# Kernel optimization log

Measured on AMD Instinct MI355X. Metric: run time of the kernel, lower is better.

## Reference

```python
import jax, jax.numpy as jnp
import numpy as np
import math

B, S, D, H = 4, 2048, 1024, 16
DH = D // H
NEG = -1e10


def setup_inputs() -> dict:
    key = jax.random.key(0)
    k1, k2, k3 = jax.random.split(key, 3)
    x = jax.random.normal(k1, (B, S, D), dtype=jnp.float32)
    # torch nn.Linear weights have shape (out_features, in_features); y = x @ W.T + b
    w1 = jax.random.normal(k2, (3 * D, D), dtype=jnp.float32) * (1.0 / math.sqrt(D))
    b1 = jnp.zeros((3 * D,), dtype=jnp.float32)
    w2 = jax.random.normal(k3, (D, D), dtype=jnp.float32) * (1.0 / math.sqrt(D))
    b2 = jnp.zeros((D,), dtype=jnp.float32)
    return {"x": x, "w1": w1, "b1": b1, "w2": w2, "b2": b2}


def reference(x, w1, b1, w2, b2):
    b, s, d = x.shape
    h, dh = H, d // H
    qkv = x @ w1.T + b1                                  # [B,S,3D]
    q, k, v = jnp.split(qkv, 3, axis=-1)                 # each [B,S,D]
    def heads(t):
        return t.reshape(b, s, h, dh).transpose(0, 2, 1, 3)  # [B,H,S,dh]
    q, k, v = heads(q), heads(k), heads(v)
    # additive causal mask: (1 - tril) * -1e10, as in the original
    mask = (1.0 - jnp.tril(jnp.ones((s, s), dtype=x.dtype))) * NEG
    scores = jnp.einsum('bhqd,bhkd->bhqk', q, k) / math.sqrt(dh) + mask
    attn = jax.nn.softmax(scores, axis=-1)
    o = jnp.einsum('bhqk,bhkd->bhqd', attn, v)           # [B,H,S,dh]
    o = o.transpose(0, 2, 1, 3).reshape(b, s, d)         # [B,S,D]
    return o @ w2.T + b2
```

## Files before the change

### kernel.cpp

```cpp
#include <hip/hip_runtime.h>
#include <stdint.h>


typedef __bf16 bf16;
typedef __attribute__((ext_vector_type(4))) __bf16 bf16x4;
typedef __attribute__((ext_vector_type(8))) __bf16 bf16x8;
typedef __attribute__((ext_vector_type(4))) float f32x4;

#define MFMA16(a, b, c) __builtin_amdgcn_mfma_f32_16x16x32_bf16((a), (b), (c), 0, 0, 0)

#if __has_builtin(__builtin_amdgcn_exp2f)
#define EXP2F(x) __builtin_amdgcn_exp2f(x)
#else
#define EXP2F(x) exp2f(x)
#endif

#define GLOAD_LDS16(gp, lp)                                                    \
  __builtin_amdgcn_global_load_lds(                                            \
      (__attribute__((address_space(1))) void*)(gp),                           \
      (__attribute__((address_space(3))) void*)(lp), 16, 0, 0)

#define SB   2048
#define D3   3072
#define DD   1024
#define QSCALE 0.18033688011112042f

__global__ __launch_bounds__(256) void cast_bf16_kernel(
    const float* __restrict__ in, bf16* __restrict__ out, int n4) {
  int stride = gridDim.x * blockDim.x;
  for (int i = blockIdx.x * blockDim.x + threadIdx.x; i < n4; i += stride) {
    float4 v = ((const float4*)in)[i];
    bf16x4 p;
    p[0] = (bf16)v.x; p[1] = (bf16)v.y; p[2] = (bf16)v.z; p[3] = (bf16)v.w;
    *(bf16x4*)(out + (size_t)i * 4) = p;
  }
}

template <int OUTMODE>
__global__ __launch_bounds__(256) void gemm_bt_kernel(
    const bf16* __restrict__ A, const bf16* __restrict__ Bw,
    const float* __restrict__ bias, void* __restrict__ Cout,
    int M, int N, int K) {
  __shared__ __attribute__((aligned(16))) bf16 At[128 * 32];
  __shared__ __attribute__((aligned(16))) bf16 Bt[128 * 32];
  const int tid = threadIdx.x;
  const int w = tid >> 6, l = tid & 63;
  const int c = l & 15, g = l >> 4;
  const int wm = w >> 1, wn = w & 1;
  const int m0 = blockIdx.y * 128, n0 = blockIdx.x * 128;

  const int srow = w * 32 + (l >> 2);
  const int scol = (l & 3) * 8;
  const bf16* Ag = A + (size_t)(m0 + srow) * K + scol;
  const bf16* Bg = Bw + (size_t)(n0 + srow) * K + scol;
  char* AtB = (char*)At + w * 2048;
  char* BtB = (char*)Bt + w * 2048;

  f32x4 acc[4][4] = {};

  for (int k0 = 0; k0 < K; k0 += 32) {
    GLOAD_LDS16(Ag + k0,            AtB);
    GLOAD_LDS16(Ag + 16 * K + k0,   AtB + 1024);
    GLOAD_LDS16(Bg + k0,            BtB);
    GLOAD_LDS16(Bg + 16 * K + k0,   BtB + 1024);
    __syncthreads();

    bf16x8 aF[4], bF[4];
    const char* Ard = (const char*)At + (wm * 64 + c) * 64 + g * 16;
    const char* Brd = (const char*)Bt + (wn * 64 + c) * 64 + g * 16;
#pragma unroll
    for (int mi = 0; mi < 4; ++mi) aF[mi] = *(const bf16x8*)(Ard + mi * 1024);
#pragma unroll
    for (int ni = 0; ni < 4; ++ni) bF[ni] = *(const bf16x8*)(Brd + ni * 1024);
#pragma unroll
    for (int mi = 0; mi < 4; ++mi)
#pragma unroll
      for (int ni = 0; ni < 4; ++ni)
        acc[mi][ni] = MFMA16(aF[mi], bF[ni], acc[mi][ni]);
    __syncthreads();
  }

#pragma unroll
  for (int ni = 0; ni < 4; ++ni) {
    const int col = n0 + wn * 64 + ni * 16 + c;
    const float bv = bias[col];
#pragma unroll
    for (int mi = 0; mi < 4; ++mi) {
      const int row = m0 + wm * 64 + mi * 16 + 4 * g;
#pragma unroll
      for (int r = 0; r < 4; ++r) {
        float v = acc[mi][ni][r] + bv;
        if (OUTMODE == 1) {
          if (col < DD) v *= QSCALE;
          ((bf16*)Cout)[(size_t)(row + r) * N + col] = (bf16)v;
        } else {
          ((float*)Cout)[(size_t)(row + r) * N + col] = v;
        }
      }
    }
  }
}

__global__ __launch_bounds__(256) void vtrans_kernel(
    const bf16* __restrict__ qkv, bf16* __restrict__ vT) {
  __shared__ __attribute__((aligned(16))) bf16 tt[64 * 72];
  const int tid = threadIdx.x;
  const int bh = blockIdx.x >> 5, st = blockIdx.x & 31;
  const int b = bh >> 4, h = bh & 15;
  const int s0 = st * 64;
  const int sr = tid >> 3, c0 = (tid & 7) * 8;
#pragma unroll
  for (int i = 0; i < 2; ++i) {
    const int srr = sr + i * 32;
    bf16x8 v = *(const bf16x8*)(qkv + (size_t)(b * SB + s0 + srr) * D3 + 2 * DD + h * 64 + c0);
    *(bf16x8*)(&tt[srr * 72 + c0]) = v;
  }
  __syncthreads();
  const int d = tid >> 2;
#pragma unroll
  for (int i = 0; i < 2; ++i) {
    const int sc = (tid & 3) * 2 + i;
    bf16x8 v;
#pragma unroll
    for (int j = 0; j < 8; ++j) v[j] = tt[(sc * 8 + j) * 72 + d];
    *(bf16x8*)(vT + (size_t)(bh * 64 + d) * SB + s0 + sc * 8) = v;
  }
}

__global__ __launch_bounds__(256, 2) void attn_kernel(
    const bf16* __restrict__ qkv, const bf16* __restrict__ vT,
    bf16* __restrict__ o) {
  __shared__ __attribute__((aligned(16))) bf16 Kt[2][128 * 64];
  __shared__ __attribute__((aligned(16))) bf16 Vt[2][64 * 128];
  const int tid = threadIdx.x;
  const int w = tid >> 6, l = tid & 63;
  const int c = l & 15, g = l >> 4;
  const int pair = blockIdx.x >> 6, bh = blockIdx.x & 63;
  const int b = bh >> 4, h = bh & 15;
  const int qtA = pair, qtB = 15 - pair;
  const int swz = (c & 7) << 4;

  const bf16* qg = qkv + (size_t)(b * SB) * D3 + h * 64;

  auto stage = [&](int kt, int buf) {
#pragma unroll
    for (int j = 0; j < 4; ++j) {
      const int row = w * 32 + j * 8 + (l >> 3);
      const int cs = ((l & 7) ^ (row & 7)) << 3;
      GLOAD_LDS16(qkv + (size_t)(b * SB + kt * 128 + row) * D3 + DD + h * 64 + cs,
                  (char*)&Kt[buf][0] + w * 4096 + j * 1024);
    }
#pragma unroll
    for (int j = 0; j < 4; ++j) {
      const int row = w * 16 + j * 4 + (l >> 4);
      const int cs = ((l & 15) ^ (row & 7)) << 3;
      GLOAD_LDS16(vT + (size_t)(bh * 64 + row) * SB + kt * 128 + cs,
                  (char*)&Vt[buf][0] + w * 4096 + j * 1024);
    }
  };

  stage(0, 0);

  bf16x8 qfA[2][2], qfB[2][2];
#pragma unroll
  for (int mi = 0; mi < 2; ++mi)
#pragma unroll
    for (int dk = 0; dk < 2; ++dk) {
      qfA[mi][dk] = *(const bf16x8*)(qg + (size_t)(qtA * 128 + w * 32 + mi * 16 + c) * D3 + dk * 32 + g * 8);
      qfB[mi][dk] = *(const bf16x8*)(qg + (size_t)(qtB * 128 + w * 32 + mi * 16 + c) * D3 + dk * 32 + g * 8);
    }

  f32x4 ofA[2][4] = {}, ofB[2][4] = {};
  float mA[2] = {-1e30f, -1e30f}, lA[2] = {0.f, 0.f};
  float mB[2] = {-1e30f, -1e30f}, lB[2] = {0.f, 0.f};
  const f32x4 zero = {0.f, 0.f, 0.f, 0.f};

  auto process = [&](int kt, int qt, int buf, bf16x8 (&qf)[2][2], float (&m)[2],
                     float (&lsum)[2], f32x4 (&of)[2][4]) {
    f32x4 sf[2][8];
#pragma unroll
    for (int f = 0; f < 8; ++f) {
      const char* kr = (const char*)&Kt[buf][0] + (f * 16 + c) * 128;
      bf16x8 kb0 = *(const bf16x8*)(kr + ((g * 16) ^ swz));
      bf16x8 kb1 = *(const bf16x8*)(kr + ((64 + g * 16) ^ swz));
#pragma unroll
      for (int mi = 0; mi < 2; ++mi) {
        f32x4 t = MFMA16(kb0, qf[mi][0], zero);
        sf[mi][f] = MFMA16(kb1, qf[mi][1], t);
      }
    }

    if (kt == qt) {
#pragma unroll
      for (int mi = 0; mi < 2; ++mi) {
        const int qloc = w * 32 + mi * 16 + c;
#pragma unroll
        for (int f = 0; f < 8; ++f)
#pragma unroll
          for (int r = 0; r < 4; ++r)
            if (f * 16 + 4 * g + r > qloc) sf[mi][f][r] = -1e30f;
      }
    }

    bf16x8 pa[2][4];
#pragma unroll
    for (int mi = 0; mi < 2; ++mi) {
      float pm = -1e30f;
#pragma unroll
      for (int f = 0; f < 8; ++f)
#pragma unroll
        for (int r = 0; r < 4; ++r) pm = fmaxf(pm, sf[mi][f][r]);
      pm = fmaxf(pm, __shfl_xor(pm, 16, 64));
      pm = fmaxf(pm, __shfl_xor(pm, 32, 64));
      if (__any(pm > m[mi] + 8.f)) {
        const float mnew = fmaxf(m[mi], pm);
        const float sc = EXP2F(m[mi] - mnew);
        m[mi] = mnew;
        lsum[mi] *= sc;
#pragma unroll
        for (int di = 0; di < 4; ++di) of[mi][di] *= sc;
      }
      float rs = 0.f;
#pragma unroll
      for (int f = 0; f < 8; ++f)
#pragma unroll
        for (int r = 0; r < 4; ++r) {
          const float pv = EXP2F(sf[mi][f][r] - m[mi]);
          sf[mi][f][r] = pv;
          rs += pv;
        }
      rs += __shfl_xor(rs, 16, 64);
      rs += __shfl_xor(rs, 32, 64);
      lsum[mi] += rs;
#pragma unroll
      for (int t = 0; t < 4; ++t)
#pragma unroll
        for (int s = 0; s < 4; ++s) {
          pa[mi][t][s]     = (bf16)sf[mi][2 * t][s];
          pa[mi][t][4 + s] = (bf16)sf[mi][2 * t + 1][s];
        }
    }

#pragma unroll
    for (int di = 0; di < 4; ++di) {
      const char* vrow = (const char*)&Vt[buf][0] + (di * 16 + c) * 256;
#pragma unroll
      for (int t = 0; t < 4; ++t) {
        bf16x4 v1 = *(const bf16x4*)(vrow + ((64 * t + 8 * g) ^ swz));
        bf16x4 v2 = *(const bf16x4*)(vrow + ((64 * t + 32 + 8 * g) ^ swz));
        bf16x8 va;
#pragma unroll
        for (int s = 0; s < 4; ++s) { va[s] = v1[s]; va[4 + s] = v2[s]; }
#pragma unroll
        for (int mi = 0; mi < 2; ++mi)
          of[mi][di] = MFMA16(va, pa[mi][t], of[mi][di]);
      }
    }
  };

  __syncthreads();

  int buf = 0;
  for (int kt = 0; kt <= qtB; ++kt) {
    if (kt < qtB) stage(kt + 1, buf ^ 1);
    if (kt <= qtA) process(kt, qtA, buf, qfA, mA, lA, ofA);
    process(kt, qtB, buf, qfB, mB, lB, ofB);
    __syncthreads();
    buf ^= 1;
  }

  auto store_tile = [&](int qt, float (&lsum)[2], f32x4 (&of)[2][4]) {
#pragma unroll
    for (int mi = 0; mi < 2; ++mi) {
      const float inv = 1.0f / lsum[mi];
      const size_t row = (size_t)(b * SB + qt * 128 + w * 32 + mi * 16 + c);
#pragma unroll
      for (int di = 0; di < 4; ++di) {
        bf16x4 st;
#pragma unroll
        for (int r = 0; r < 4; ++r) st[r] = (bf16)(of[mi][di][r] * inv);
        *(bf16x4*)(o + row * DD + h * 64 + di * 16 + 4 * g) = st;
      }
    }
  };
  store_tile(qtA, lA, ofA);
  store_tile(qtB, lB, ofB);
}

extern "C" void kernel_launch(void* const* d_in, const int* in_sizes, int n_in,
                              void* d_out, int out_size, void* d_ws, size_t ws_size,
                              hipStream_t stream) {
  const float* x  = (const float*)d_in[0];
  const float* w1 = (const float*)d_in[1];
  const float* b1 = (const float*)d_in[2];
  const float* w2 = (const float*)d_in[3];
  const float* b2 = (const float*)d_in[4];
  float* out = (float*)d_out;

  bf16* xb   = (bf16*)d_ws;
  bf16* w1b  = xb   + (size_t)8  * 1024 * 1024;
  bf16* w2b  = w1b  + (size_t)3  * 1024 * 1024;
  bf16* qkvb = w2b  + (size_t)1  * 1024 * 1024;
  bf16* vT   = qkvb + (size_t)8192 * 3072;
  bf16* ob   = vT   + (size_t)8  * 1024 * 1024;

  cast_bf16_kernel<<<2048, 256, 0, stream>>>(x,  xb,  (8 * 1024 * 1024) / 4);
  cast_bf16_kernel<<<768,  256, 0, stream>>>(w1, w1b, (3 * 1024 * 1024) / 4);
  cast_bf16_kernel<<<256,  256, 0, stream>>>(w2, w2b, (1 * 1024 * 1024) / 4);

  gemm_bt_kernel<1><<<dim3(24, 64), 256, 0, stream>>>(xb, w1b, b1, qkvb, 8192, 3072, 1024);
  vtrans_kernel<<<2048, 256, 0, stream>>>(qkvb, vT);
  attn_kernel<<<512, 256, 0, stream>>>(qkvb, vT, ob);
  gemm_bt_kernel<0><<<dim3(8, 64), 256, 0, stream>>>(ob, w2b, b2, out, 8192, 1024, 1024);
}
```

Baseline: 185.2 us.

## Replace GEMM with 256x256 tile, 8-wave, double-buffered swizzled LDS pipeline

Rewrites both projection GEMMs as a 256x256-tile kernel with 8 waves and double-buffered, XOR-swizzled LDS. The next K-tiles are loaded directly into LDS in quarter steps interleaved with the MFMA work, using explicit waitcnt and barriers and raised wave priority during the MFMAs. Block indices are remapped to improve L2 locality. This cuts per-tile global traffic and exposed load latency, but uses much more LDS and registers. The output GEMM then launches only 128 blocks, which may underfill the GPU.

New measurement: 200.6 us. 8.3% more time.

```diff
diff --git a/kernel.cpp b/kernel.cpp
--- a/kernel.cpp
+++ b/kernel.cpp
@@ -37,59 +37,101 @@
 }
 
 template <int OUTMODE>
-__global__ __launch_bounds__(256) void gemm_bt_kernel(
+__global__ __launch_bounds__(512, 2) void gemm8p_kernel(
     const bf16* __restrict__ A, const bf16* __restrict__ Bw,
     const float* __restrict__ bias, void* __restrict__ Cout,
-    int M, int N, int K) {
-  __shared__ __attribute__((aligned(16))) bf16 At[128 * 32];
-  __shared__ __attribute__((aligned(16))) bf16 Bt[128 * 32];
+    int M, int N, int K, int NBn) {
+  __shared__ __attribute__((aligned(16))) bf16 As[2][256 * 64];
+  __shared__ __attribute__((aligned(16))) bf16 Bs[2][256 * 64];
   const int tid = threadIdx.x;
   const int w = tid >> 6, l = tid & 63;
   const int c = l & 15, g = l >> 4;
-  const int wm = w >> 1, wn = w & 1;
-  const int m0 = blockIdx.y * 128, n0 = blockIdx.x * 128;
-
-  const int srow = w * 32 + (l >> 2);
-  const int scol = (l & 3) * 8;
-  const bf16* Ag = A + (size_t)(m0 + srow) * K + scol;
-  const bf16* Bg = Bw + (size_t)(n0 + srow) * K + scol;
-  char* AtB = (char*)At + w * 2048;
-  char* BtB = (char*)Bt + w * 2048;
-
-  f32x4 acc[4][4] = {};
-
-  for (int k0 = 0; k0 < K; k0 += 32) {
-    GLOAD_LDS16(Ag + k0,            AtB);
-    GLOAD_LDS16(Ag + 16 * K + k0,   AtB + 1024);
-    GLOAD_LDS16(Bg + k0,            BtB);
-    GLOAD_LDS16(Bg + 16 * K + k0,   BtB + 1024);
-    __syncthreads();
-
-    bf16x8 aF[4], bF[4];
-    const char* Ard = (const char*)At + (wm * 64 + c) * 64 + g * 16;
-    const char* Brd = (const char*)Bt + (wn * 64 + c) * 64 + g * 16;
-#pragma unroll
-    for (int mi = 0; mi < 4; ++mi) aF[mi] = *(const bf16x8*)(Ard + mi * 1024);
-#pragma unroll
-    for (int ni = 0; ni < 4; ++ni) bF[ni] = *(const bf16x8*)(Brd + ni * 1024);
-#pragma unroll
-    for (int mi = 0; mi < 4; ++mi)
-#pragma unroll
-      for (int ni = 0; ni < 4; ++ni)
-        acc[mi][ni] = MFMA16(aF[mi], bF[ni], acc[mi][ni]);
-    __syncthreads();
-  }
-
-#pragma unroll
-  for (int ni = 0; ni < 4; ++ni) {
-    const int col = n0 + wn * 64 + ni * 16 + c;
-    const float bv = bias[col];
-#pragma unroll
-    for (int mi = 0; mi < 4; ++mi) {
-      const int row = m0 + wm * 64 + mi * 16 + 4 * g;
+  const int wm = w >> 2, wn = w & 3;
+  const int nwg = gridDim.x;
+  const int sw = ((int)blockIdx.x % 8) * (nwg / 8) + (int)blockIdx.x / 8;
+  const int bn = sw % NBn, bm = sw / NBn;
+  const int m0 = bm * 256, n0 = bn * 256;
+  const int NT = K >> 6;
+
+  const int srow_w = l >> 3;
+  const int scol = ((l & 7) ^ srow_w) << 3;
+
+  auto stage = [&](int op, int h, int buf, int kt) {
+    if (kt > NT - 1) kt = NT - 1;
+    const int rbase = h * 128 + w * 8 + srow_w;
+    const bf16* src = (op == 0) ? (A + (size_t)(m0 + rbase) * K)
+                                : (Bw + (size_t)(n0 + rbase) * K);
+    char* dst = (char*)((op == 0) ? &As[buf][0] : &Bs[buf][0]) + h * 16384 + w * 1024;
+#pragma unroll
+    for (int ld = 0; ld < 2; ++ld)
+      GLOAD_LDS16(src + (size_t)(ld * 64) * K + kt * 64 + scol, dst + ld * 8192);
+  };
+
+  stage(0, 0, 0, 0); stage(0, 1, 0, 0); stage(1, 0, 0, 0); stage(1, 1, 0, 0);
+  stage(0, 0, 1, 1); stage(0, 1, 1, 1); stage(1, 0, 1, 1); stage(1, 1, 1, 1);
+  asm volatile("s_waitcnt vmcnt(8)" ::: "memory");
+  __builtin_amdgcn_s_barrier();
+  __builtin_amdgcn_sched_barrier(0);
+
+  f32x4 acc[8][4] = {};
+
+  for (int it = 0; it < (NT >> 1); ++it) {
+#pragma unroll
+    for (int tp = 0; tp < 2; ++tp) {
+      const int T = 2 * it + tp;
+#pragma unroll
+      for (int q = 0; q < 4; ++q) {
+        const int qm = q >> 1, qn = q & 1;
+        bf16x8 aF[4][2], bF[2][2];
+#pragma unroll
+        for (int mf = 0; mf < 4; ++mf)
+#pragma unroll
+          for (int ks = 0; ks < 2; ++ks) {
+            const int r = qm * 128 + wm * 64 + mf * 16 + c;
+            aF[mf][ks] = *(const bf16x8*)((const char*)&As[tp][0] + r * 128 +
+                                          (((ks * 4 + g) ^ (r & 7)) << 4));
+          }
+#pragma unroll
+        for (int nf = 0; nf < 2; ++nf)
+#pragma unroll
+          for (int ks = 0; ks < 2; ++ks) {
+            const int r = qn * 128 + wn * 32 + nf * 16 + c;
+            bF[nf][ks] = *(const bf16x8*)((const char*)&Bs[tp][0] + r * 128 +
+                                          (((ks * 4 + g) ^ (r & 7)) << 4));
+          }
+        if (q == 0)      stage(0, 1, tp ^ 1, T + 1);
+        else if (q == 1) stage(1, 1, tp ^ 1, T + 1);
+        else if (q == 2) stage(0, 0, tp,     T + 2);
+        else             stage(1, 0, tp,     T + 2);
+        __builtin_amdgcn_s_barrier();
+        __builtin_amdgcn_sched_barrier(0);
+        __builtin_amdgcn_s_setprio(1);
+#pragma unroll
+        for (int mf = 0; mf < 4; ++mf)
+#pragma unroll
+          for (int nf = 0; nf < 2; ++nf)
+#pragma unroll
+            for (int ks = 0; ks < 2; ++ks)
+              acc[qm * 4 + mf][qn * 2 + nf] =
+                  MFMA16(aF[mf][ks], bF[nf][ks], acc[qm * 4 + mf][qn * 2 + nf]);
+        __builtin_amdgcn_s_setprio(0);
+        if (q == 3) asm volatile("s_waitcnt vmcnt(4)" ::: "memory");
+        __builtin_amdgcn_s_barrier();
+        __builtin_amdgcn_sched_barrier(0);
+      }
+    }
+  }
+
+#pragma unroll
+  for (int im = 0; im < 8; ++im) {
+    const int row = m0 + (im >> 2) * 128 + wm * 64 + (im & 3) * 16 + 4 * g;
+#pragma unroll
+    for (int in_ = 0; in_ < 4; ++in_) {
+      const int col = n0 + (in_ >> 1) * 128 + wn * 32 + (in_ & 1) * 16 + c;
+      const float bv = bias[col];
 #pragma unroll
       for (int r = 0; r < 4; ++r) {
-        float v = acc[mi][ni][r] + bv;
+        float v = acc[im][in_][r] + bv;
         if (OUTMODE == 1) {
           if (col < DD) v *= QSCALE;
           ((bf16*)Cout)[(size_t)(row + r) * N + col] = (bf16)v;
@@ -308,8 +350,8 @@
   cast_bf16_kernel<<<768,  256, 0, stream>>>(w1, w1b, (3 * 1024 * 1024) / 4);
   cast_bf16_kernel<<<256,  256, 0, stream>>>(w2, w2b, (1 * 1024 * 1024) / 4);
 
-  gemm_bt_kernel<1><<<dim3(24, 64), 256, 0, stream>>>(xb, w1b, b1, qkvb, 8192, 3072, 1024);
+  gemm8p_kernel<1><<<384, 512, 0, stream>>>(xb, w1b, b1, qkvb, 8192, 3072, 1024, 12);
   vtrans_kernel<<<2048, 256, 0, stream>>>(qkvb, vT);
   attn_kernel<<<512, 256, 0, stream>>>(qkvb, vT, ob);
-  gemm_bt_kernel<0><<<dim3(8, 64), 256, 0, stream>>>(ob, w2b, b2, out, 8192, 1024, 1024);
-}
+  gemm8p_kernel<0><<<128, 512, 0, stream>>>(ob, w2b, b2, out, 8192, 1024, 1024, 4);
+}
```

## Rewrite projection GEMMs with double-buffered LDS, 32x32 MFMA, swizzle and XCD remap

Applied to the files above, without the earlier changes.

Replaces the single-buffered 128x128x32 GEMM with a double-buffered 128x128x64 pipeline. The next K tile is prefetched into LDS while MFMAs run on the current one, using 32x32x16 bf16 MFMAs and an XOR-swizzled LDS layout to avoid bank conflicts. Blocks are remapped round-robin across XCDs for L2 locality, and s_setprio is raised around the MFMA bursts. This aims to hide global load latency and halve the barrier count per K, at the cost of more LDS (64KB per block) and register pressure.

After: 174.8 us. -5.6%, faster.

```diff
diff --git a/kernel.cpp b/kernel.cpp
--- a/kernel.cpp
+++ b/kernel.cpp
@@ -6,8 +6,10 @@
 typedef __attribute__((ext_vector_type(4))) __bf16 bf16x4;
 typedef __attribute__((ext_vector_type(8))) __bf16 bf16x8;
 typedef __attribute__((ext_vector_type(4))) float f32x4;
+typedef __attribute__((ext_vector_type(16))) float f32x16;
 
 #define MFMA16(a, b, c) __builtin_amdgcn_mfma_f32_16x16x32_bf16((a), (b), (c), 0, 0, 0)
+#define MFMA32(a, b, c) __builtin_amdgcn_mfma_f32_32x32x16_bf16((a), (b), (c), 0, 0, 0)
 
 #if __has_builtin(__builtin_amdgcn_exp2f)
 #define EXP2F(x) __builtin_amdgcn_exp2f(x)
@@ -37,64 +39,95 @@
 }
 
 template <int OUTMODE>
-__global__ __launch_bounds__(256) void gemm_bt_kernel(
+__global__ __launch_bounds__(256, 2) void gemm2p_kernel(
     const bf16* __restrict__ A, const bf16* __restrict__ Bw,
     const float* __restrict__ bias, void* __restrict__ Cout,
-    int M, int N, int K) {
-  __shared__ __attribute__((aligned(16))) bf16 At[128 * 32];
-  __shared__ __attribute__((aligned(16))) bf16 Bt[128 * 32];
+    int M, int N, int K, int NBn) {
+  __shared__ __attribute__((aligned(16))) bf16 As[2][128 * 64];
+  __shared__ __attribute__((aligned(16))) bf16 Bs[2][128 * 64];
   const int tid = threadIdx.x;
   const int w = tid >> 6, l = tid & 63;
-  const int c = l & 15, g = l >> 4;
+  const int lr = l & 31, lh = l >> 5;
   const int wm = w >> 1, wn = w & 1;
-  const int m0 = blockIdx.y * 128, n0 = blockIdx.x * 128;
-
-  const int srow = w * 32 + (l >> 2);
-  const int scol = (l & 3) * 8;
-  const bf16* Ag = A + (size_t)(m0 + srow) * K + scol;
-  const bf16* Bg = Bw + (size_t)(n0 + srow) * K + scol;
-  char* AtB = (char*)At + w * 2048;
-  char* BtB = (char*)Bt + w * 2048;
-
-  f32x4 acc[4][4] = {};
-
-  for (int k0 = 0; k0 < K; k0 += 32) {
-    GLOAD_LDS16(Ag + k0,            AtB);
-    GLOAD_LDS16(Ag + 16 * K + k0,   AtB + 1024);
-    GLOAD_LDS16(Bg + k0,            BtB);
-    GLOAD_LDS16(Bg + 16 * K + k0,   BtB + 1024);
+  const int nwg = gridDim.x;
+  const int sw = ((int)blockIdx.x % 8) * (nwg / 8) + (int)blockIdx.x / 8;
+  const int bn = sw % NBn, bm = sw / NBn;
+  const int m0 = bm * 128, n0 = bn * 128;
+  const int NT = K >> 6;
+
+  const int srow = l >> 3;
+  const int scol = ((l & 7) ^ srow) << 3;
+
+  auto stage = [&](int buf, int kt) {
+#pragma unroll
+    for (int j = 0; j < 4; ++j) {
+      const int rb = j * 32 + w * 8 + srow;
+      GLOAD_LDS16(A + (size_t)(m0 + rb) * K + kt * 64 + scol,
+                  (char*)&As[buf][0] + j * 4096 + w * 1024);
+      GLOAD_LDS16(Bw + (size_t)(n0 + rb) * K + kt * 64 + scol,
+                  (char*)&Bs[buf][0] + j * 4096 + w * 1024);
+    }
+  };
+
+  auto ldA = [&](int buf, int ks, bf16x8 (&aF)[2]) {
+#pragma unroll
+    for (int ti = 0; ti < 2; ++ti) {
+      const int r = wm * 64 + ti * 32 + lr;
+      aF[ti] = *(const bf16x8*)((const char*)&As[buf][0] + r * 128 +
+                                (((ks * 2 + lh) ^ (lr & 7)) << 4));
+    }
+  };
+  auto ldB = [&](int buf, int ks, bf16x8 (&bF)[2]) {
+#pragma unroll
+    for (int tj = 0; tj < 2; ++tj) {
+      const int r = wn * 64 + tj * 32 + lr;
+      bF[tj] = *(const bf16x8*)((const char*)&Bs[buf][0] + r * 128 +
+                                (((ks * 2 + lh) ^ (lr & 7)) << 4));
+    }
+  };
+
+  f32x16 acc[2][2] = {};
+  auto domfma = [&](bf16x8 (&aF)[2], bf16x8 (&bF)[2]) {
+    __builtin_amdgcn_s_setprio(1);
+#pragma unroll
+    for (int ti = 0; ti < 2; ++ti)
+#pragma unroll
+      for (int tj = 0; tj < 2; ++tj)
+        acc[ti][tj] = MFMA32(aF[ti], bF[tj], acc[ti][tj]);
+    __builtin_amdgcn_s_setprio(0);
+  };
+
+  stage(0, 0);
+  __syncthreads();
+
+  for (int T = 0; T < NT; ++T) {
+    const int buf = T & 1;
+    if (T + 1 < NT) stage(buf ^ 1, T + 1);
+    bf16x8 aP[2], bP[2], aQ[2], bQ[2];
+    ldA(buf, 0, aP); ldB(buf, 0, bP);
+    ldA(buf, 1, aQ); ldB(buf, 1, bQ); domfma(aP, bP);
+    ldA(buf, 2, aP); ldB(buf, 2, bP); domfma(aQ, bQ);
+    ldA(buf, 3, aQ); ldB(buf, 3, bQ); domfma(aP, bP);
+    domfma(aQ, bQ);
     __syncthreads();
-
-    bf16x8 aF[4], bF[4];
-    const char* Ard = (const char*)At + (wm * 64 + c) * 64 + g * 16;
-    const char* Brd = (const char*)Bt + (wn * 64 + c) * 64 + g * 16;
-#pragma unroll
-    for (int mi = 0; mi < 4; ++mi) aF[mi] = *(const bf16x8*)(Ard + mi * 1024);
-#pragma unroll
-    for (int ni = 0; ni < 4; ++ni) bF[ni] = *(const bf16x8*)(Brd + ni * 1024);
-#pragma unroll
-    for (int mi = 0; mi < 4; ++mi)
-#pragma unroll
-      for (int ni = 0; ni < 4; ++ni)
-        acc[mi][ni] = MFMA16(aF[mi], bF[ni], acc[mi][ni]);
-    __syncthreads();
-  }
-
-#pragma unroll
-  for (int ni = 0; ni < 4; ++ni) {
-    const int col = n0 + wn * 64 + ni * 16 + c;
-    const float bv = bias[col];
-#pragma unroll
-    for (int mi = 0; mi < 4; ++mi) {
-      const int row = m0 + wm * 64 + mi * 16 + 4 * g;
-#pragma unroll
-      for (int r = 0; r < 4; ++r) {
-        float v = acc[mi][ni][r] + bv;
+  }
+
+#pragma unroll
+  for (int ti = 0; ti < 2; ++ti) {
+    const int r0 = m0 + wm * 64 + ti * 32 + 4 * lh;
+#pragma unroll
+    for (int tj = 0; tj < 2; ++tj) {
+      const int col = n0 + wn * 64 + tj * 32 + lr;
+      const float bv = bias[col];
+#pragma unroll
+      for (int e = 0; e < 16; ++e) {
+        const int row = r0 + (e & 3) + 8 * (e >> 2);
+        float v = acc[ti][tj][e] + bv;
         if (OUTMODE == 1) {
           if (col < DD) v *= QSCALE;
-          ((bf16*)Cout)[(size_t)(row + r) * N + col] = (bf16)v;
+          ((bf16*)Cout)[(size_t)row * N + col] = (bf16)v;
         } else {
-          ((float*)Cout)[(size_t)(row + r) * N + col] = v;
+          ((float*)Cout)[(size_t)row * N + col] = v;
         }
       }
     }
@@ -308,8 +341,8 @@
   cast_bf16_kernel<<<768,  256, 0, stream>>>(w1, w1b, (3 * 1024 * 1024) / 4);
   cast_bf16_kernel<<<256,  256, 0, stream>>>(w2, w2b, (1 * 1024 * 1024) / 4);
 
-  gemm_bt_kernel<1><<<dim3(24, 64), 256, 0, stream>>>(xb, w1b, b1, qkvb, 8192, 3072, 1024);
+  gemm2p_kernel<1><<<1536, 256, 0, stream>>>(xb, w1b, b1, qkvb, 8192, 3072, 1024, 24);
   vtrans_kernel<<<2048, 256, 0, stream>>>(qkvb, vT);
   attn_kernel<<<512, 256, 0, stream>>>(qkvb, vT, ob);
-  gemm_bt_kernel<0><<<dim3(8, 64), 256, 0, stream>>>(ob, w2b, b2, out, 8192, 1024, 1024);
-}
+  gemm2p_kernel<0><<<512, 256, 0, stream>>>(ob, w2b, b2, out, 8192, 1024, 1024, 8);
+}
```
